# Performance work log

Hardware: AMD Instinct MI355X
Metric: run time of the kernel (lower is better)

The kernel has to match this reference:

```python
import jax, jax.numpy as jnp
import numpy as np

B, T, C, U = 16, 128, 64, 128
ODE_UNFOLDS = 6
EPS = 1e-8


def setup_inputs() -> dict:
    key = jax.random.key(0)
    ks = jax.random.split(key, 12)
    u = lambda k, s, lo, hi: jax.random.uniform(k, s, jnp.float32, lo, hi)
    return dict(
        x=jax.random.normal(ks[0], (B, T, C), jnp.float32),
        h0=jnp.zeros((B, U), jnp.float32),
        gleak=u(ks[1], (U,), 0.001, 1.0),
        vleak=u(ks[2], (U,), -0.2, 0.2),
        cm=u(ks[3], (U,), 0.4, 0.6),
        sigma=u(ks[4], (U, U), 3.0, 8.0),
        mu=u(ks[5], (U, U), 0.3, 0.8),
        w=u(ks[6], (U, U), 0.001, 1.0),
        erev=jnp.sign(jax.random.normal(ks[7], (U, U))).astype(jnp.float32),
        sensory_sigma=u(ks[8], (C, U), 3.0, 8.0),
        sensory_mu=u(ks[9], (C, U), 0.3, 0.8),
        sensory_w=u(ks[10], (C, U), 0.001, 1.0),
        sensory_erev=jnp.sign(jax.random.normal(ks[11], (C, U))).astype(jnp.float32),
        input_w=jnp.ones((C,), jnp.float32),
        input_b=jnp.zeros((C,), jnp.float32),
        output_w=jnp.ones((U,), jnp.float32),
        output_b=jnp.zeros((U,), jnp.float32),
    )


def reference(x, h0, gleak, vleak, cm, sigma, mu, w, erev,
              sensory_sigma, sensory_mu, sensory_w, sensory_erev,
              input_w, input_b, output_w, output_b):
    sp = jax.nn.softplus
    # Positive-constrained params (implicit_param_constraints=True)
    w_pos = sp(w)                      # [U,U]
    sw_pos = sp(sensory_w)             # [C,U]
    gl = sp(gleak)                     # [U]
    # elapsed_time ts = 1.0 -> cm_t = softplus(cm) / (1/ode_unfolds)
    cm_t = sp(cm) * ODE_UNFOLDS        # [U]

    def step(h, xt):
        # input affine mapping
        xt = xt * input_w + input_b                                        # [B,C]
        # sensory synapses (constant across unfolds)
        sens_act = sw_pos * jax.nn.sigmoid(sensory_sigma * (xt[:, :, None] - sensory_mu))  # [B,C,U]
        w_num_s = jnp.sum(sens_act * sensory_erev, axis=1)                 # [B,U]
        w_den_s = jnp.sum(sens_act, axis=1)                                # [B,U]
        v = h
        for _ in range(ODE_UNFOLDS):
            # recurrent synapses: pre dim 1, post dim 2
            w_act = w_pos * jax.nn.sigmoid(sigma * (v[:, :, None] - mu))   # [B,U,U]
            w_num = jnp.sum(w_act * erev, axis=1) + w_num_s                # [B,U]
            w_den = jnp.sum(w_act, axis=1) + w_den_s                       # [B,U]
            num = cm_t * v + gl * vleak + w_num
            den = cm_t + gl + w_den
            v = num / (den + EPS)
        out = v * output_w + output_b   # motor_size == units for FullyConnected
        return v, out

    h_final, outs = jax.lax.scan(step, h0, jnp.swapaxes(x, 0, 1))  # outs: [T,B,U]
    readout = jnp.swapaxes(outs, 0, 1)                             # [B,T,U]
    return readout, h_final
```

## Files before the change

kernel.cpp:

```cpp
#include <hip/hip_runtime.h>

#define NB 16
#define NT 128
#define NC 64
#define NU 128
#define UNFOLDS 6
#define LTC_EPS 1e-8f
#define LOG2E 1.44269504088896340736f
#define LN2   0.69314718055994530942f

typedef float f32x2 __attribute__((ext_vector_type(2)));

__device__ __forceinline__ float fast_softplus(float x) {
    return LN2 * __builtin_amdgcn_logf(1.0f + __builtin_amdgcn_exp2f(x * LOG2E));
}

template<int CTRL>
__device__ __forceinline__ float qperm(float x) {
    return __int_as_float(__builtin_amdgcn_update_dpp(
        0, __float_as_int(x), CTRL, 0xF, 0xF, true));
}
__device__ __forceinline__ float sum8(float x) {
    x += qperm<0xB1>(x);
    x += qperm<0x4E>(x);
    x += qperm<0x141>(x);
    return x;
}

__global__ __launch_bounds__(128)
void ltc_sens_kernel(const float* __restrict__ x,
                     const float* __restrict__ ssigma,
                     const float* __restrict__ smu,
                     const float* __restrict__ sw,
                     const float* __restrict__ serev,
                     const float* __restrict__ iw,
                     const float* __restrict__ ib,
                     float2* __restrict__ sens)
{
    __shared__ float xt[NC];
    const int blk = blockIdx.x;
    const int b = blk >> 7;
    const int t = blk & (NT - 1);
    const int j = threadIdx.x;
    if (j < NC) xt[j] = fmaf(x[(b * NT + t) * NC + j], iw[j], ib[j]);
    __syncthreads();

    float n0 = 0.f, n1 = 0.f, d0 = 0.f, d1 = 0.f;
#pragma unroll 8
    for (int c = 0; c < NC; ++c) {
        const int idx = c * NU + j;
        float sg = ssigma[idx];
        float m  = smu[idx];
        float wp = fast_softplus(sw[idx]);
        float er = serev[idx];
        float tt = (m - xt[c]) * (sg * LOG2E);
        float e  = __builtin_amdgcn_exp2f(tt);
        float r  = __builtin_amdgcn_rcpf(1.0f + e);
        float wr = wp * r;
        if (c & 1) { n1 = fmaf(wr, er, n1); d1 += wr; }
        else       { n0 = fmaf(wr, er, n0); d0 += wr; }
    }
    sens[(b * NT + t) * NU + j] = make_float2(n0 + n1, d0 + d1);
}

__global__ __launch_bounds__(1024, 4)
void ltc_seq_kernel(const float* __restrict__ h0,
                    const float* __restrict__ gleak,
                    const float* __restrict__ vleak,
                    const float* __restrict__ cm,
                    const float* __restrict__ sigma,
                    const float* __restrict__ mu,
                    const float* __restrict__ w,
                    const float* __restrict__ erev,
                    const float* __restrict__ ow,
                    const float* __restrict__ ob,
                    const float2* __restrict__ sens,
                    float* __restrict__ out)
{
    __shared__ __align__(16) float v_lds[2][NU];

    const int tid = threadIdx.x;
    const int b   = blockIdx.x;
    const int j   = tid >> 3;
    const int k   = tid & 7;

    f32x2 rA2[8], rB2[8], rW2[8], aW2[8];
#pragma unroll
    for (int q = 0; q < 8; ++q) {
        const int g   = (q + k) & 7;
        const int i0  = (k << 4) + (g << 1);
        const int id0 = i0 * NU + j;
        const int id1 = id0 + NU;
        const float sg0 = sigma[id0], sg1 = sigma[id1];
        const float m0  = mu[id0],    m1  = mu[id1];
        const float wp0 = fast_softplus(w[id0]), wp1 = fast_softplus(w[id1]);
        const float er0 = erev[id0],  er1 = erev[id1];
        f32x2 a;  a.x = -sg0 * LOG2E;  a.y = -sg1 * LOG2E;
        f32x2 bb; bb.x = -a.x * m0;    bb.y = -a.y * m1;
        f32x2 ww; ww.x = wp0 * er0;    ww.y = wp1 * er1;
        f32x2 aw; aw.x = wp0;          aw.y = wp1;
        rA2[q] = a; rB2[q] = bb; rW2[q] = ww; aW2[q] = aw;
    }

    const float cmt    = 6.0f * fast_softplus(cm[j]);
    const float gl     = fast_softplus(gleak[j]);
    const float glv    = gl * vleak[j];
    const float cmt_gl = cmt + gl + LTC_EPS;
    const float owj    = ow[j];
    const float obj    = ob[j];
    float vj = h0[b * NU + j];
    if (k == 0) v_lds[0][j] = vj;
    __syncthreads();

    int p = 0;
    float2 s_cur = sens[b * NT * NU + j];

    for (int t = 0; t < NT; ++t) {
#pragma unroll
        for (int q = 0; q < 8; ++q) {
            asm volatile("" : "+v"(rA2[q]), "+v"(rB2[q]), "+v"(rW2[q]), "+v"(aW2[q]));
        }

        const float snum = s_cur.x;
        const float sden = s_cur.y;
        const int tn = (t + 1 < NT) ? (t + 1) : t;
        const float2 s_next = sens[(b * NT + tn) * NU + j];

#pragma unroll
        for (int u = 0; u < UNFOLDS; ++u) {
            f32x2 n2 = {0.f, 0.f};
            f32x2 d2 = {0.f, 0.f};
#pragma unroll
            for (int q = 0; q < 8; ++q) {
                const int g = (q + k) & 7;
                const f32x2 v2 = *(const f32x2*)&v_lds[p][(k << 4) + (g << 1)];
                f32x2 t2 = rA2[q] * v2 + rB2[q];
                f32x2 e2;
                e2.x = __builtin_amdgcn_exp2f(t2.x);
                e2.y = __builtin_amdgcn_exp2f(t2.y);
                f32x2 u2 = e2 + (f32x2){1.0f, 1.0f};
                f32x2 r2;
                r2.x = __builtin_amdgcn_rcpf(u2.x);
                r2.y = __builtin_amdgcn_rcpf(u2.y);
                n2 = rW2[q] * r2 + n2;
                d2 = aW2[q] * r2 + d2;
            }
            const float wn = sum8(n2.x + n2.y) + snum;
            const float wd = sum8(d2.x + d2.y) + sden;
            const float numf = fmaf(cmt, vj, glv) + wn;
            const float denf = cmt_gl + wd;
            vj = numf * __builtin_amdgcn_rcpf(denf);
            if (k == 0) v_lds[p ^ 1][j] = vj;
            __syncthreads();
            p ^= 1;
        }

        if (k == 0) out[(b * NT + t) * NU + j] = fmaf(vj, owj, obj);
        s_cur = s_next;
    }
    if (k == 0) out[NB * NT * NU + b * NU + j] = vj;
}

extern "C" void kernel_launch(void* const* d_in, const int* in_sizes, int n_in,
                              void* d_out, int out_size, void* d_ws, size_t ws_size,
                              hipStream_t stream) {
    const float* x      = (const float*)d_in[0];
    const float* h0     = (const float*)d_in[1];
    const float* gleak  = (const float*)d_in[2];
    const float* vleak  = (const float*)d_in[3];
    const float* cm     = (const float*)d_in[4];
    const float* sigma  = (const float*)d_in[5];
    const float* mu     = (const float*)d_in[6];
    const float* w      = (const float*)d_in[7];
    const float* erev   = (const float*)d_in[8];
    const float* ssig   = (const float*)d_in[9];
    const float* smu    = (const float*)d_in[10];
    const float* sw     = (const float*)d_in[11];
    const float* serev  = (const float*)d_in[12];
    const float* iw     = (const float*)d_in[13];
    const float* ibv    = (const float*)d_in[14];
    const float* ow     = (const float*)d_in[15];
    const float* ob     = (const float*)d_in[16];
    float* out = (float*)d_out;

    float2* sens = (float2*)d_ws;
    ltc_sens_kernel<<<NB * NT, 128, 0, stream>>>(x, ssig, smu, sw, serev, iw, ibv, sens);
    ltc_seq_kernel<<<NB, 1024, 0, stream>>>(h0, gleak, vleak, cm, sigma, mu, w, erev,
                                            ow, ob, (const float2*)sens, out);
}
```

Before: 748.8 us.

## Batch four sigmoid reciprocals into one rcp and fold bias terms into sums

The inner recurrent loop now computes four sigmoid denominators and replaces four reciprocal instructions with a single rcp plus a few multiplies, using the product trick. It also reads v as float4 from LDS with a rotation over groups of four. The sensory and leak constants are pre-split by 1/8 and seeded into the lane accumulators, so they come out of the 8-lane reduction and the post-reduction adds go away. The product of four (1+e) terms can overflow fp32 when the exp2 arguments are large, which risks inf/NaN or lost precision for saturated sigmoids.

Measured after the change: 783.3 us. 4.6% more time.

```diff
diff --git a/kernel.cpp b/kernel.cpp
--- a/kernel.cpp
+++ b/kernel.cpp
@@ -86,20 +86,24 @@
 
     f32x2 rA2[8], rB2[8], rW2[8], aW2[8];
 #pragma unroll
-    for (int q = 0; q < 8; ++q) {
-        const int g   = (q + k) & 7;
-        const int i0  = (k << 4) + (g << 1);
-        const int id0 = i0 * NU + j;
-        const int id1 = id0 + NU;
-        const float sg0 = sigma[id0], sg1 = sigma[id1];
-        const float m0  = mu[id0],    m1  = mu[id1];
-        const float wp0 = fast_softplus(w[id0]), wp1 = fast_softplus(w[id1]);
-        const float er0 = erev[id0],  er1 = erev[id1];
-        f32x2 a;  a.x = -sg0 * LOG2E;  a.y = -sg1 * LOG2E;
-        f32x2 bb; bb.x = -a.x * m0;    bb.y = -a.y * m1;
-        f32x2 ww; ww.x = wp0 * er0;    ww.y = wp1 * er1;
-        f32x2 aw; aw.x = wp0;          aw.y = wp1;
-        rA2[q] = a; rB2[q] = bb; rW2[q] = ww; aW2[q] = aw;
+    for (int m = 0; m < 4; ++m) {
+        const int rot = (m + k) & 3;
+#pragma unroll
+        for (int h = 0; h < 2; ++h) {
+            const int c   = 2 * m + h;
+            const int i0  = (k << 4) + (rot << 2) + 2 * h;
+            const int id0 = i0 * NU + j;
+            const int id1 = id0 + NU;
+            const float sg0 = sigma[id0], sg1 = sigma[id1];
+            const float m0  = mu[id0],    m1  = mu[id1];
+            const float wp0 = fast_softplus(w[id0]), wp1 = fast_softplus(w[id1]);
+            const float er0 = erev[id0],  er1 = erev[id1];
+            f32x2 a;  a.x = -sg0 * LOG2E;  a.y = -sg1 * LOG2E;
+            f32x2 bb; bb.x = -a.x * m0;    bb.y = -a.y * m1;
+            f32x2 ww; ww.x = wp0 * er0;    ww.y = wp1 * er1;
+            f32x2 aw; aw.x = wp0;          aw.y = wp1;
+            rA2[c] = a; rB2[c] = bb; rW2[c] = ww; aW2[c] = aw;
+        }
     }
 
     const float cmt    = 6.0f * fast_softplus(cm[j]);
@@ -121,35 +125,48 @@
             asm volatile("" : "+v"(rA2[q]), "+v"(rB2[q]), "+v"(rW2[q]), "+v"(aW2[q]));
         }
 
-        const float snum = s_cur.x;
-        const float sden = s_cur.y;
+        const float nb = 0.125f * (s_cur.x + glv);
+        const float db = 0.125f * (s_cur.y + cmt_gl);
         const int tn = (t + 1 < NT) ? (t + 1) : t;
         const float2 s_next = sens[(b * NT + tn) * NU + j];
 
 #pragma unroll
         for (int u = 0; u < UNFOLDS; ++u) {
-            f32x2 n2 = {0.f, 0.f};
-            f32x2 d2 = {0.f, 0.f};
-#pragma unroll
-            for (int q = 0; q < 8; ++q) {
-                const int g = (q + k) & 7;
-                const f32x2 v2 = *(const f32x2*)&v_lds[p][(k << 4) + (g << 1)];
-                f32x2 t2 = rA2[q] * v2 + rB2[q];
-                f32x2 e2;
-                e2.x = __builtin_amdgcn_exp2f(t2.x);
-                e2.y = __builtin_amdgcn_exp2f(t2.y);
-                f32x2 u2 = e2 + (f32x2){1.0f, 1.0f};
-                f32x2 r2;
-                r2.x = __builtin_amdgcn_rcpf(u2.x);
-                r2.y = __builtin_amdgcn_rcpf(u2.y);
-                n2 = rW2[q] * r2 + n2;
-                d2 = aW2[q] * r2 + d2;
+            f32x2 n2 = {nb, 0.f};
+            f32x2 d2 = {db, 0.f};
+#pragma unroll
+            for (int m = 0; m < 4; ++m) {
+                const float4 vv = *(const float4*)&v_lds[p][(k << 4) + (((m + k) & 3) << 2)];
+                const f32x2 v0 = {vv.x, vv.y};
+                const f32x2 v1 = {vv.z, vv.w};
+                const f32x2 t0 = rA2[2 * m] * v0 + rB2[2 * m];
+                const f32x2 t1 = rA2[2 * m + 1] * v1 + rB2[2 * m + 1];
+                f32x2 e0, e1;
+                e0.x = __builtin_amdgcn_exp2f(t0.x);
+                e0.y = __builtin_amdgcn_exp2f(t0.y);
+                e1.x = __builtin_amdgcn_exp2f(t1.x);
+                e1.y = __builtin_amdgcn_exp2f(t1.y);
+                const f32x2 one = {1.0f, 1.0f};
+                const f32x2 u0 = e0 + one;
+                const f32x2 u1 = e1 + one;
+                const float p01 = u0.x * u0.y;
+                const float p23 = u1.x * u1.y;
+                const float rall = __builtin_amdgcn_rcpf(p01 * p23);
+                const float r01 = rall * p23;
+                const float r23 = rall * p01;
+                const f32x2 rr0 = {r01, r01};
+                const f32x2 rr1 = {r23, r23};
+                const f32x2 r0 = rr0 * __builtin_shufflevector(u0, u0, 1, 0);
+                const f32x2 r1 = rr1 * __builtin_shufflevector(u1, u1, 1, 0);
+                n2 = rW2[2 * m] * r0 + n2;
+                n2 = rW2[2 * m + 1] * r1 + n2;
+                d2 = aW2[2 * m] * r0 + d2;
+                d2 = aW2[2 * m + 1] * r1 + d2;
             }
-            const float wn = sum8(n2.x + n2.y) + snum;
-            const float wd = sum8(d2.x + d2.y) + sden;
-            const float numf = fmaf(cmt, vj, glv) + wn;
-            const float denf = cmt_gl + wd;
-            vj = numf * __builtin_amdgcn_rcpf(denf);
+            const float wn = sum8(n2.x + n2.y);
+            const float wd = sum8(d2.x + d2.y);
+            const float numf = fmaf(cmt, vj, wn);
+            vj = numf * __builtin_amdgcn_rcpf(wd);
             if (k == 0) v_lds[p ^ 1][j] = vj;
             __syncthreads();
             p ^= 1;
```
